# Optimization experiments

Hardware: AMD Instinct MI355X
Metric: run time of the kernel (lower is better)

Reference implementation:

```python
import jax, jax.numpy as jnp
import numpy as np

B = 128          # batch of IQ signals
L = 128          # signal length
PL = 16          # patch length
ST = 4           # patch stride
WIN = 4          # local window
NPATCH = (L - PL) // ST + 1   # 29
HID = 256
NCLS = 8
NG = B * NPATCH               # number of patch graphs
N = NG * PL                   # total nodes


def _build_edges():
    src, dst = [], []
    for i in range(PL):
        for j in range(PL):
            if 0 < abs(i - j) <= WIN:
                src.append(i); dst.append(j)
    bs = np.array(src, np.int32)          # [108]
    bd = np.array(dst, np.int32)
    off = (np.arange(NG, dtype=np.int32) * PL)[:, None]
    isrc = (off + bs[None, :]).reshape(-1)
    idst = (off + bd[None, :]).reshape(-1)
    # cross-patch edges: last node of patch p -> first node of patch p+1
    b = np.arange(B, dtype=np.int32)[:, None]
    p = np.arange(NPATCH - 1, dtype=np.int32)[None, :]
    csrc = (b * NPATCH * PL + p * PL + (PL - 1)).reshape(-1)
    cdst = (b * NPATCH * PL + (p + 1) * PL).reshape(-1)
    return np.concatenate([isrc, csrc]), np.concatenate([idst, cdst])


def setup_inputs() -> dict:
    key = jax.random.key(0)
    ks = jax.random.split(key, 10)
    s = 0.05
    esrc, edst = _build_edges()
    return {
        "iq_signal": jax.random.normal(ks[0], (B, 2, L), jnp.float32),
        "edge_src": jnp.asarray(esrc),
        "edge_dst": jnp.asarray(edst),
        # SAGEConv layer 0 (in=2): lin_l (agg, with bias), lin_r (root, no bias)
        "W0_agg": jax.random.normal(ks[1], (HID, 2), jnp.float32) * s,
        "W0_root": jax.random.normal(ks[2], (HID, 2), jnp.float32) * s,
        "b0": jnp.zeros((HID,), jnp.float32),
        # SAGEConv layers 1..3 (256 -> 256), stacked
        "W_agg": jax.random.normal(ks[3], (3, HID, HID), jnp.float32) * s,
        "W_root": jax.random.normal(ks[4], (3, HID, HID), jnp.float32) * s,
        "b_lin": jnp.zeros((3, HID), jnp.float32),
        # per-layer LayerNorms
        "ln_scale": jnp.ones((4, HID), jnp.float32),
        "ln_bias": jnp.zeros((4, HID), jnp.float32),
        # classifier head
        "cls_W1": jax.random.normal(ks[5], (HID, HID), jnp.float32) * s,
        "cls_b1": jnp.zeros((HID,), jnp.float32),
        "cls_ln_scale": jnp.ones((HID,), jnp.float32),
        "cls_ln_bias": jnp.zeros((HID,), jnp.float32),
        "cls_W2": jax.random.normal(ks[6], (NCLS, HID), jnp.float32) * s,
        "cls_b2": jnp.zeros((NCLS,), jnp.float32),
    }


def _ln(x, g, b):
    m = x.mean(-1, keepdims=True)
    v = ((x - m) ** 2).mean(-1, keepdims=True)
    return (x - m) * jax.lax.rsqrt(v + 1e-5) * g + b


def reference(iq_signal, edge_src, edge_dst, W0_agg, W0_root, b0,
              W_agg, W_root, b_lin, ln_scale, ln_bias,
              cls_W1, cls_b1, cls_ln_scale, cls_ln_bias, cls_W2, cls_b2):
    # patch extraction: [B,2,L] -> [B,NPATCH,PL,2] -> node features [N,2]
    idx = jnp.arange(NPATCH)[:, None] * ST + jnp.arange(PL)[None, :]   # [29,16]
    x = jnp.transpose(iq_signal[:, :, idx], (0, 2, 3, 1)).reshape(-1, 2)

    # in-degree for mean aggregation (0 -> safe divide by 1)
    ones = jnp.ones((edge_dst.shape[0],), x.dtype)
    deg = jax.ops.segment_sum(ones, edge_dst, num_segments=N)
    inv_deg = 1.0 / jnp.maximum(deg, 1.0)

    def sage(h, Wa, Wr, b):
        # mean-aggregate neighbor messages, then lin_l(agg) + lin_r(h) + bias
        agg = jax.ops.segment_sum(h[edge_src], edge_dst, num_segments=N)
        agg = agg * inv_deg[:, None]
        return agg @ Wa.T + h @ Wr.T + b

    # layer 0 (2 -> 256): no residual (shape change)
    h = jax.nn.relu(_ln(sage(x, W0_agg, W0_root, b0), ln_scale[0], ln_bias[0]))
    # layers 1..3 with residual
    for l in range(3):
        hn = jax.nn.relu(_ln(sage(h, W_agg[l], W_root[l], b_lin[l]),
                             ln_scale[l + 1], ln_bias[l + 1]))
        h = h + hn

    node_emb = h                                  # [N, 256]
    # global_mean_pool per patch graph (16 consecutive nodes each)
    gf = node_emb.reshape(NG, PL, HID).mean(axis=1)   # [NG, 256]
    z = jax.nn.relu(_ln(gf @ cls_W1.T + cls_b1, cls_ln_scale, cls_ln_bias))
    logits = z @ cls_W2.T + cls_b2                # [NG, 8]
    return logits, gf, node_emb
```

## Files before the change

kernel.cpp:

```cpp
#include <hip/hip_runtime.h>
#include <hip/hip_bf16.h>

typedef __hip_bfloat16 bf16;
typedef unsigned short u16;
typedef unsigned int uint32;
typedef __attribute__((ext_vector_type(8))) short bf16x8;
typedef __attribute__((ext_vector_type(4))) float f32x4;

#define BATCH   128
#define LSIG    128
#define PL      16
#define ST      4
#define WIN     4
#define NPATCH  29
#define NG      (BATCH * NPATCH)
#define NNODE   (NG * PL)
#define HID     256
#define NCLS    8

#define IQ_OFF    0
#define W0A_OFF   32768
#define W0R_OFF   33280
#define B0_OFF    33792
#define BLIN_OFF  34048
#define LNS_OFF   34816
#define LNB_OFF   35840
#define W1T_OFF   36864
#define CB1_OFF   102400
#define CLNS_OFF  102656
#define CLNB_OFF  102912
#define CW2_OFF   103168
#define CB2_OFF   105216
#define CVT_TOTAL 105224
#define WB_TOTAL  393216

#define P_BYTE_OFF   4096
#define WB_BYTE_OFF  425984
#define A_BYTE_OFF   1216512
#define B_BYTE_OFF   1959936
#define GF_EOFF      (NG * NCLS)
#define EMB_EOFF     (NG * NCLS + NG * HID)

#define MFMA_BF16 __builtin_amdgcn_mfma_f32_16x16x32_bf16

__device__ __forceinline__ float b2f(bf16 x) { return __bfloat162float(x); }
__device__ __forceinline__ float lof(uint32 u) { return __uint_as_float(u << 16); }
__device__ __forceinline__ float hif(uint32 u) { return __uint_as_float(u & 0xFFFF0000u); }
__device__ __forceinline__ uint32 packbf(float a, float b) {
  bf16 r0 = __float2bfloat16(a), r1 = __float2bfloat16(b);
  return ((uint32)(*(const u16*)&r1) << 16) | (uint32)(*(const u16*)&r0);
}
__device__ __forceinline__ float ldmix(const void* p, size_t i, int fl) {
  return fl ? ((const float*)p)[i] : __bfloat162float(((const bf16*)p)[i]);
}
__device__ __forceinline__ void gl_lds16(const uint32* gsrc, uint32* ldst) {
  __builtin_amdgcn_global_load_lds(
      (const __attribute__((address_space(1))) uint32*)gsrc,
      (__attribute__((address_space(3))) uint32*)ldst, 16, 0, 0);
}

__global__ __launch_bounds__(256) void detect_kernel(const u16* __restrict__ iq, int* flag) {
  __shared__ int sbig, snz;
  int t = threadIdx.x;
  if (t == 0) { sbig = 0; snz = 0; }
  __syncthreads();
  int big = 0, nz = 0;
  for (int e = t; e < 16384; e += 256) {
    u16 u = iq[2 * e];
    int ex = (u >> 7) & 0xFF;
    if (ex >= 0xC0) big++;
    if (u != 0) nz++;
  }
  atomicAdd(&sbig, big); atomicAdd(&snz, nz);
  __syncthreads();
  if (t == 0) *flag = (sbig > 4 || snz < 100) ? 1 : 0;
}

__global__ __launch_bounds__(256) void convert_all(
    const int* __restrict__ flag,
    const void* iq, const void* w0a, const void* w0r, const void* b0,
    const void* blin, const void* lns, const void* lnb,
    const void* cw1, const void* cb1, const void* clns, const void* clnb,
    const void* cw2, const void* cb2,
    const void* wag, const void* wro,
    float* __restrict__ P, bf16* __restrict__ WB) {
  int idx = blockIdx.x * 256 + threadIdx.x;
  int fl = *flag;
  if (idx < CVT_TOTAL) {
    float v;
    if (idx < W0A_OFF)        v = ldmix(iq,  idx, fl);
    else if (idx < W0R_OFF)   v = ldmix(w0a, idx - W0A_OFF, fl);
    else if (idx < B0_OFF)    v = ldmix(w0r, idx - W0R_OFF, fl);
    else if (idx < BLIN_OFF)  v = ldmix(b0,  idx - B0_OFF, fl);
    else if (idx < LNS_OFF)   v = ldmix(blin, idx - BLIN_OFF, fl);
    else if (idx < LNB_OFF)   v = ldmix(lns, idx - LNS_OFF, fl);
    else if (idx < W1T_OFF)   v = ldmix(lnb, idx - LNB_OFF, fl);
    else if (idx < CB1_OFF) { int t2 = idx - W1T_OFF;
      v = ldmix(cw1, (t2 & 255) * 256 + (t2 >> 8), fl); }
    else if (idx < CLNS_OFF)  v = ldmix(cb1, idx - CB1_OFF, fl);
    else if (idx < CLNB_OFF)  v = ldmix(clns, idx - CLNS_OFF, fl);
    else if (idx < CW2_OFF)   v = ldmix(clnb, idx - CLNB_OFF, fl);
    else if (idx < CB2_OFF)   v = ldmix(cw2, idx - CW2_OFF, fl);
    else                      v = ldmix(cb2, idx - CB2_OFF, fl);
    P[idx] = v;
  } else if (idx < CVT_TOTAL + WB_TOTAL) {
    int k = idx - CVT_TOTAL;
    int l = k >> 17, m = (k >> 16) & 1, r = k & 65535;
    const void* src = m ? wro : wag;
    WB[k] = __float2bfloat16(ldmix(src, l * 65536 + r, fl));
  }
}

__global__ __launch_bounds__(256) void layer0_kernel(
    const float* __restrict__ P, bf16* __restrict__ hout) {
  int g = blockIdx.x, f = threadIdx.x;
  int b = g / NPATCH, p = g % NPATCH;
  __shared__ float x_s[PL][2];
  __shared__ float xp_s[2];
  __shared__ float agg_s[PL][2];
  __shared__ float o_s[PL][HID];
  __shared__ float mv_s[PL][2];
  if (f < 32) { int j = f & 15, c = f >> 4;
    x_s[j][c] = P[IQ_OFF + (b * 2 + c) * LSIG + p * ST + j]; }
  if (f < 2) xp_s[f] = (p > 0) ? P[IQ_OFF + (b * 2 + f) * LSIG + (p - 1) * ST + PL - 1] : 0.f;
  __syncthreads();
  if (f < 32) { int j = f & 15, c = f >> 4;
    float s = 0.f;
    int lo = j - WIN < 0 ? 0 : j - WIN, hi = j + WIN > 15 ? 15 : j + WIN;
    for (int i = lo; i <= hi; ++i) if (i != j) s += x_s[i][c];
    int deg = (j < WIN ? j : WIN) + ((15 - j) < WIN ? (15 - j) : WIN);
    if (j == 0 && p > 0) { s += xp_s[c]; deg += 1; }
    agg_s[j][c] = s / (float)deg;
  }
  __syncthreads();
  float wa0 = P[W0A_OFF + f * 2], wa1 = P[W0A_OFF + f * 2 + 1];
  float wr0 = P[W0R_OFF + f * 2], wr1 = P[W0R_OFF + f * 2 + 1];
  float bb = P[B0_OFF + f];
#pragma unroll
  for (int j = 0; j < PL; ++j)
    o_s[j][f] = agg_s[j][0] * wa0 + agg_s[j][1] * wa1 + x_s[j][0] * wr0 + x_s[j][1] * wr1 + bb;
  __syncthreads();
  { int j = f >> 4, q = f & 15;
    float s = 0.f, s2 = 0.f;
#pragma unroll
    for (int i = 0; i < 16; ++i) { float v = o_s[j][q + 16 * i]; s += v; s2 += v * v; }
#pragma unroll
    for (int m = 8; m >= 1; m >>= 1) { s += __shfl_xor(s, m); s2 += __shfl_xor(s2, m); }
    if (q == 0) { float mean = s * (1.f / HID);
      float var = s2 * (1.f / HID) - mean * mean;
      mv_s[j][0] = mean; mv_s[j][1] = rsqrtf(var + 1e-5f); }
  }
  __syncthreads();
  float gl = P[LNS_OFF + f], bl = P[LNB_OFF + f];
#pragma unroll
  for (int j = 0; j < PL; ++j) {
    float v = (o_s[j][f] - mv_s[j][0]) * mv_s[j][1] * gl + bl;
    v = v > 0.f ? v : 0.f;
    bf16 x = __float2bfloat16(v);
    ((u16*)hout)[(size_t)(g * PL + j) * 256 + ((((f >> 3) ^ (j & 7))) << 3) + (f & 7)] = *(const u16*)&x;
  }
}

template<int LAST>
__global__ __launch_bounds__(256, 2) void sage_mfma(
    const bf16* __restrict__ hin,
    const bf16* __restrict__ Wa, const bf16* __restrict__ Wr,
    const float* __restrict__ bias,
    const float* __restrict__ lng, const float* __restrict__ lnb,
    bf16* __restrict__ hout,
    void* __restrict__ dout, const int* __restrict__ flag) {
  int t = threadIdx.x;
  int w = t >> 6, l = t & 63, lr = l & 15, lg = l >> 4;
  int g0 = blockIdx.x * 4;
  size_t nbase = (size_t)g0 * PL;
  __shared__ uint32 h32[64 * 128];
  __shared__ uint32 a32[64 * 128];
  float* mvp = (float*)h32;
  const uint32* hinw = (const uint32*)hin;

  int colbase = w * 64;
  const bf16* waB = Wa + (colbase + lr) * HID + lg * 8;
  const bf16* wrB = Wr + (colbase + lr) * HID + lg * 8;
  bf16x8 wa0[2][8], wr0[2][8];
#pragma unroll
  for (int nt = 0; nt < 2; ++nt)
#pragma unroll
    for (int ks = 0; ks < 8; ++ks) {
      wa0[nt][ks] = *(const bf16x8*)(waB + nt * 16 * HID + ks * 32);
      wr0[nt][ks] = *(const bf16x8*)(wrB + nt * 16 * HID + ks * 32);
    }

  const uint32* hgw = hinw + nbase * 128;
#pragma unroll
  for (int it = 0; it < 8; ++it) {
    int off = (it * 4 + w) * 256;
    gl_lds16(hgw + off + (l << 2), &h32[off]);
  }
  __syncthreads();

  {
    int c2 = t & 127, Ph = t >> 7;
#pragma unroll
    for (int pi = 0; pi < 2; ++pi) {
      int pp = Ph + pi * 2;
      int pr = pp * 16;
      int hp = ((g0 + pp) % NPATCH) != 0;
      float vlo[16], vhi[16];
#pragma unroll
      for (int j = 0; j < 16; ++j) {
        uint32 u = h32[(pr + j) * 128 + (((c2 >> 2) ^ (j & 7)) << 2) + (c2 & 3)];
        vlo[j] = lof(u); vhi[j] = hif(u);
      }
      float blo = 0.f, bhi = 0.f;
      if (hp) {
        uint32 u;
        if (pp == 0) u = hinw[(nbase - 1) * 128 + (((c2 >> 2) ^ 7) << 2) + (c2 & 3)];
        else { int br = pr - 1;
          u = h32[br * 128 + (((c2 >> 2) ^ (br & 7)) << 2) + (c2 & 3)]; }
        blo = lof(u); bhi = hif(u);
      }
#pragma unroll
      for (int j = 0; j < 16; ++j) {
        const int a = (j - WIN < 0) ? 0 : j - WIN;
        const int b = (j + WIN > 15) ? 15 : j + WIN;
        float slo = 0.f, shi = 0.f;
#pragma unroll
        for (int i = 0; i < 16; ++i)
          if (i >= a && i <= b && i != j) { slo += vlo[i]; shi += vhi[i]; }
        float deg = (float)((j < WIN ? j : WIN) + (15 - j < WIN ? 15 - j : WIN));
        if (j == 0 && hp) { slo += blo; shi += bhi; deg += 1.f; }
        float inv = 1.f / deg;
        a32[(pr + j) * 128 + (((c2 >> 2) ^ (j & 7)) << 2) + (c2 & 3)] = packbf(slo * inv, shi * inv);
      }
    }
  }
  __syncthreads();

  f32x4 acc[4][4];
#pragma unroll
  for (int m = 0; m < 4; ++m)
#pragma unroll
    for (int n = 0; n < 4; ++n) acc[m][n] = (f32x4){0.f, 0.f, 0.f, 0.f};
  __builtin_amdgcn_s_setprio(1);
#pragma unroll
  for (int ks = 0; ks < 8; ++ks) {
    bf16x8 wa1[2], wr1[2];
#pragma unroll
    for (int nt = 0; nt < 2; ++nt) {
      wa1[nt] = *(const bf16x8*)(waB + (nt + 2) * 16 * HID + ks * 32);
      wr1[nt] = *(const bf16x8*)(wrB + (nt + 2) * 16 * HID + ks * 32);
    }
#pragma unroll
    for (int m = 0; m < 4; ++m) {
      int idx = (m * 16 + lr) * 128 + (((ks * 4 + lg) ^ (lr & 7)) << 2);
      bf16x8 af = *(const bf16x8*)&a32[idx];
      bf16x8 hf = *(const bf16x8*)&h32[idx];
      acc[m][0] = MFMA_BF16(af, wa0[0][ks], acc[m][0], 0, 0, 0);
      acc[m][0] = MFMA_BF16(hf, wr0[0][ks], acc[m][0], 0, 0, 0);
      acc[m][1] = MFMA_BF16(af, wa0[1][ks], acc[m][1], 0, 0, 0);
      acc[m][1] = MFMA_BF16(hf, wr0[1][ks], acc[m][1], 0, 0, 0);
      acc[m][2] = MFMA_BF16(af, wa1[0],     acc[m][2], 0, 0, 0);
      acc[m][2] = MFMA_BF16(hf, wr1[0],     acc[m][2], 0, 0, 0);
      acc[m][3] = MFMA_BF16(af, wa1[1],     acc[m][3], 0, 0, 0);
      acc[m][3] = MFMA_BF16(hf, wr1[1],     acc[m][3], 0, 0, 0);
    }
  }
  __builtin_amdgcn_s_setprio(0);
#pragma unroll
  for (int nt = 0; nt < 4; ++nt) {
    float bv = bias[colbase + nt * 16 + lr];
#pragma unroll
    for (int m = 0; m < 4; ++m) {
      acc[m][nt][0] += bv; acc[m][nt][1] += bv; acc[m][nt][2] += bv; acc[m][nt][3] += bv;
    }
  }
  __syncthreads();

#pragma unroll
  for (int m = 0; m < 4; ++m)
#pragma unroll
    for (int nt = 0; nt < 4; ++nt) {
      int col = colbase + nt * 16 + lr;
#pragma unroll
      for (int r = 0; r < 4; ++r) {
        int row = m * 16 + lg * 4 + r;
        int i16 = row * 256 + (((col >> 3) ^ (row & 7)) << 3) + (col & 7);
        bf16 x = __float2bfloat16(acc[m][nt][r]);
        ((u16*)a32)[i16] = *(const u16*)&x;
      }
    }
  __syncthreads();

  {
    int row = t >> 2, q = t & 3;
    float s = 0.f, s2 = 0.f;
#pragma unroll
    for (int i = 0; i < 32; ++i) {
      int d = q * 32 + i;
      uint32 u = a32[row * 128 + (((d >> 2) ^ (row & 7)) << 2) + (d & 3)];
      float a = lof(u), b = hif(u);
      s += a + b; s2 += a * a + b * b;
    }
    s += __shfl_xor(s, 1); s2 += __shfl_xor(s2, 1);
    s += __shfl_xor(s, 2); s2 += __shfl_xor(s2, 2);
    if (q == 0) { float mean = s * (1.f / HID);
      mvp[row * 2] = mean;
      mvp[row * 2 + 1] = rsqrtf(s2 * (1.f / HID) - mean * mean + 1e-5f); }
  }
  __syncthreads();

  {
    int c2 = t & 127, prt = t >> 7;
    float gl0 = lng[c2 * 2], gl1 = lng[c2 * 2 + 1];
    float bl0 = lnb[c2 * 2], bl1 = lnb[c2 * 2 + 1];
    uint32* outw = nullptr;
    if constexpr (!LAST) outw = (uint32*)hout + nbase * 128;
    const uint32* inw = hinw + nbase * 128;
    int fl = 0;
    if constexpr (LAST) fl = *flag;
#pragma unroll
    for (int pi = 0; pi < 2; ++pi) {
      float sga = 0.f, sgb = 0.f;
#pragma unroll
      for (int i = 0; i < 16; ++i) {
        int row = prt * 32 + pi * 16 + i;
        int pidx = row * 128 + (((c2 >> 2) ^ (row & 7)) << 2) + (c2 & 3);
        uint32 u = a32[pidx];
        float mean = mvp[row * 2], rstd = mvp[row * 2 + 1];
        float a = (lof(u) - mean) * rstd * gl0 + bl0; a = a > 0.f ? a : 0.f;
        float b_ = (hif(u) - mean) * rstd * gl1 + bl1; b_ = b_ > 0.f ? b_ : 0.f;
        uint32 hu = inw[pidx];
        a += lof(hu); b_ += hif(hu);
        if constexpr (!LAST) {
          outw[pidx] = packbf(a, b_);
        } else {
          sga += a; sgb += b_;
          if (fl) {
            size_t ei = (size_t)EMB_EOFF + (nbase + row) * 256 + (size_t)c2 * 2;
            *(float2*)&((float*)dout)[ei] = make_float2(a, b_);
          } else {
            ((uint32*)dout)[(EMB_EOFF >> 1) + (nbase + row) * 128 + c2] = packbf(a, b_);
          }
        }
      }
      if constexpr (LAST) {
        float ga = sga * (1.f / PL), gb = sgb * (1.f / PL);
        int gidx = g0 + prt * 2 + pi;
        if (fl) {
          size_t gi = (size_t)GF_EOFF + (size_t)gidx * 256 + (size_t)c2 * 2;
          *(float2*)&((float*)dout)[gi] = make_float2(ga, gb);
        } else {
          ((uint32*)dout)[(GF_EOFF >> 1) + gidx * 128 + c2] = packbf(ga, gb);
        }
      }
    }
  }
}

__global__ __launch_bounds__(256) void head_kernel(
    const void* __restrict__ gin, const float* __restrict__ P,
    void* __restrict__ dout, const int* __restrict__ flag) {
  int g = blockIdx.x, f = threadIdx.x;
  int fl = *flag;
  __shared__ float gf_s[HID];
  __shared__ float z_s[HID];
  __shared__ float ps[4], ps2[4];
  __shared__ float mr[2];
  gf_s[f] = fl ? ((const float*)gin)[(size_t)GF_EOFF + (size_t)g * HID + f]
               : b2f(((const bf16*)gin)[(size_t)GF_EOFF + (size_t)g * HID + f]);
  __syncthreads();
  float acc = P[CB1_OFF + f];
  for (int k = 0; k < HID; k += 4) {
    const float4 gv = *(const float4*)(&gf_s[k]);
    acc = fmaf(gv.x, P[W1T_OFF + (k + 0) * HID + f], acc);
    acc = fmaf(gv.y, P[W1T_OFF + (k + 1) * HID + f], acc);
    acc = fmaf(gv.z, P[W1T_OFF + (k + 2) * HID + f], acc);
    acc = fmaf(gv.w, P[W1T_OFF + (k + 3) * HID + f], acc);
  }
  float s1 = acc, s2 = acc * acc;
#pragma unroll
  for (int m = 32; m >= 1; m >>= 1) { s1 += __shfl_xor(s1, m); s2 += __shfl_xor(s2, m); }
  int wid = f >> 6, lane = f & 63;
  if (lane == 0) { ps[wid] = s1; ps2[wid] = s2; }
  __syncthreads();
  if (f == 0) {
    float S = ps[0] + ps[1] + ps[2] + ps[3];
    float S2 = ps2[0] + ps2[1] + ps2[2] + ps2[3];
    float mean = S * (1.f / HID);
    mr[0] = mean; mr[1] = rsqrtf(S2 * (1.f / HID) - mean * mean + 1e-5f);
  }
  __syncthreads();
  float z = (acc - mr[0]) * mr[1] * P[CLNS_OFF + f] + P[CLNB_OFF + f];
  z = z > 0.f ? z : 0.f;
  z_s[f] = z;
  __syncthreads();
  {
    int cls = f >> 5, lane2 = f & 31;
    float a = 0.f;
    for (int k = lane2; k < HID; k += 32)
      a = fmaf(z_s[k], P[CW2_OFF + cls * HID + k], a);
    a += __shfl_xor(a, 16); a += __shfl_xor(a, 8);
    a += __shfl_xor(a, 4);  a += __shfl_xor(a, 2); a += __shfl_xor(a, 1);
    if (lane2 == 0) {
      a += P[CB2_OFF + cls];
      size_t ei = (size_t)g * NCLS + cls;
      if (fl) ((float*)dout)[ei] = a; else ((bf16*)dout)[ei] = __float2bfloat16(a);
    }
  }
}

extern "C" void kernel_launch(void* const* d_in, const int* in_sizes, int n_in,
                              void* d_out, int out_size, void* d_ws, size_t ws_size,
                              hipStream_t stream) {
  char* ws = (char*)d_ws;
  int*   flag = (int*)ws;
  float* P    = (float*)(ws + P_BYTE_OFF);
  bf16*  WB   = (bf16*)(ws + WB_BYTE_OFF);
  bf16*  A    = (bf16*)(ws + A_BYTE_OFF);
  bf16*  B    = (bf16*)((char*)d_out + B_BYTE_OFF);

  detect_kernel<<<1, 256, 0, stream>>>((const u16*)d_in[0], flag);
  convert_all<<<(CVT_TOTAL + WB_TOTAL + 255) / 256, 256, 0, stream>>>(
      flag, d_in[0], d_in[3], d_in[4], d_in[5], d_in[8],
      d_in[9], d_in[10], d_in[11], d_in[12], d_in[13], d_in[14], d_in[15], d_in[16],
      d_in[6], d_in[7], P, WB);

  layer0_kernel<<<NG, 256, 0, stream>>>(P, A);
  sage_mfma<0><<<NG / 4, 256, 0, stream>>>(A, WB, WB + 65536,
      P + BLIN_OFF, P + LNS_OFF + HID, P + LNB_OFF + HID, B, nullptr, flag);
  sage_mfma<0><<<NG / 4, 256, 0, stream>>>(B, WB + 131072, WB + 131072 + 65536,
      P + BLIN_OFF + HID, P + LNS_OFF + 2 * HID, P + LNB_OFF + 2 * HID, A, nullptr, flag);
  sage_mfma<1><<<NG / 4, 256, 0, stream>>>(A, WB + 262144, WB + 262144 + 65536,
      P + BLIN_OFF + 2 * HID, P + LNS_OFF + 3 * HID, P + LNB_OFF + 3 * HID, nullptr, d_out, flag);
  head_kernel<<<NG, 256, 0, stream>>>(d_out, P, d_out, flag);
}
```

Before: 225.3 us.

## Add 8-patch-per-block SAGE kernel with in-place LDS aggregation for middle layers

Introduces a new SAGE layer kernel that processes 8 patch graphs per 512-thread block. It computes the root GEMM first, then aggregates neighbours in place in a single 64KB LDS buffer and runs the aggregation GEMM on the same buffer, instead of using separate h and agg buffers. Weight fragments are read directly from global memory/cache per MFMA. The aim is to cut LDS footprint and per-block overhead and to amortise weight reads over more rows. The trade-off is more global weight traffic per block, and 64KB of LDS per block may limit occupancy.

After: 421.8 us. 1.87x slower.

```diff
diff --git a/kernel.cpp b/kernel.cpp
--- a/kernel.cpp
+++ b/kernel.cpp
@@ -161,6 +161,144 @@
   }
 }
 
+__global__ __launch_bounds__(512, 2) void sage_bp8(
+    const bf16* __restrict__ hin,
+    const bf16* __restrict__ Wa, const bf16* __restrict__ Wr,
+    const float* __restrict__ bias,
+    const float* __restrict__ lng, const float* __restrict__ lnb,
+    bf16* __restrict__ hout) {
+  int t = threadIdx.x;
+  int w = t >> 6, l = t & 63, lr = l & 15, lg = l >> 4;
+  int g0 = blockIdx.x * 8;
+  size_t nbase = (size_t)g0 * PL;
+  __shared__ uint32 hb[128 * 128];
+  const uint32* hinw = (const uint32*)hin;
+
+  const uint32* hg = hinw + nbase * 128;
+#pragma unroll
+  for (int it = 0; it < 8; ++it) {
+    int off = (it * 8 + w) * 256;
+    gl_lds16(hg + off + (l << 2), &hb[off]);
+  }
+  __syncthreads();
+
+  int rowbase = w * 16;
+  const bf16* wrB = Wr + lr * HID + lg * 8;
+  const bf16* waB = Wa + lr * HID + lg * 8;
+
+  f32x4 acc[16];
+#pragma unroll
+  for (int n = 0; n < 16; ++n) acc[n] = (f32x4){0.f, 0.f, 0.f, 0.f};
+  __builtin_amdgcn_s_setprio(1);
+#pragma unroll
+  for (int ks = 0; ks < 8; ++ks) {
+    bf16x8 hf = *(const bf16x8*)&hb[(rowbase + lr) * 128 + (((ks * 4 + lg) ^ (lr & 7)) << 2)];
+#pragma unroll
+    for (int nt = 0; nt < 16; ++nt) {
+      bf16x8 wf = *(const bf16x8*)(wrB + nt * 16 * HID + ks * 32);
+      acc[nt] = MFMA_BF16(hf, wf, acc[nt], 0, 0, 0);
+    }
+  }
+  __builtin_amdgcn_s_setprio(0);
+
+  int c2 = t & 127, pg = t >> 7;
+  uint32 bnd[2];
+#pragma unroll
+  for (int pi2 = 0; pi2 < 2; ++pi2) {
+    int pi = pg * 2 + pi2;
+    int hp = ((g0 + pi) % NPATCH) != 0;
+    uint32 u = 0;
+    if (hp) {
+      if (pi == 0) u = hinw[(nbase - 1) * 128 + (((c2 >> 2) ^ 7) << 2) + (c2 & 3)];
+      else { int br = pi * 16 - 1;
+        u = hb[br * 128 + (((c2 >> 2) ^ 7) << 2) + (c2 & 3)]; }
+    }
+    bnd[pi2] = u;
+  }
+  __syncthreads();
+
+#pragma unroll
+  for (int pi2 = 0; pi2 < 2; ++pi2) {
+    int pi = pg * 2 + pi2;
+    int pr = pi * 16;
+    int hp = ((g0 + pi) % NPATCH) != 0;
+    float vlo[16], vhi[16];
+#pragma unroll
+    for (int j = 0; j < 16; ++j) {
+      uint32 u = hb[(pr + j) * 128 + (((c2 >> 2) ^ (j & 7)) << 2) + (c2 & 3)];
+      vlo[j] = lof(u); vhi[j] = hif(u);
+    }
+    float blo = lof(bnd[pi2]), bhi = hif(bnd[pi2]);
+#pragma unroll
+    for (int j = 0; j < 16; ++j) {
+      const int a = (j - WIN < 0) ? 0 : j - WIN;
+      const int b = (j + WIN > 15) ? 15 : j + WIN;
+      float slo = 0.f, shi = 0.f;
+#pragma unroll
+      for (int i = 0; i < 16; ++i)
+        if (i >= a && i <= b && i != j) { slo += vlo[i]; shi += vhi[i]; }
+      float deg = (float)((j < WIN ? j : WIN) + (15 - j < WIN ? 15 - j : WIN));
+      if (j == 0 && hp) { slo += blo; shi += bhi; deg += 1.f; }
+      float inv = 1.f / deg;
+      hb[(pr + j) * 128 + (((c2 >> 2) ^ (j & 7)) << 2) + (c2 & 3)] = packbf(slo * inv, shi * inv);
+    }
+  }
+  __syncthreads();
+
+  __builtin_amdgcn_s_setprio(1);
+#pragma unroll
+  for (int ks = 0; ks < 8; ++ks) {
+    bf16x8 af = *(const bf16x8*)&hb[(rowbase + lr) * 128 + (((ks * 4 + lg) ^ (lr & 7)) << 2)];
+#pragma unroll
+    for (int nt = 0; nt < 16; ++nt) {
+      bf16x8 wf = *(const bf16x8*)(waB + nt * 16 * HID + ks * 32);
+      acc[nt] = MFMA_BF16(af, wf, acc[nt], 0, 0, 0);
+    }
+  }
+  __builtin_amdgcn_s_setprio(0);
+
+#pragma unroll
+  for (int nt = 0; nt < 16; ++nt) {
+    float bv = bias[nt * 16 + lr];
+    acc[nt][0] += bv; acc[nt][1] += bv; acc[nt][2] += bv; acc[nt][3] += bv;
+  }
+  float mean[4], rstd[4];
+#pragma unroll
+  for (int r = 0; r < 4; ++r) {
+    float s = 0.f, s2 = 0.f;
+#pragma unroll
+    for (int nt = 0; nt < 16; ++nt) { float v = acc[nt][r]; s += v; s2 += v * v; }
+    s += __shfl_xor(s, 1); s2 += __shfl_xor(s2, 1);
+    s += __shfl_xor(s, 2); s2 += __shfl_xor(s2, 2);
+    s += __shfl_xor(s, 4); s2 += __shfl_xor(s2, 4);
+    s += __shfl_xor(s, 8); s2 += __shfl_xor(s2, 8);
+    mean[r] = s * (1.f / HID);
+    rstd[r] = rsqrtf(s2 * (1.f / HID) - mean[r] * mean[r] + 1e-5f);
+  }
+
+  float glv[16], blv[16];
+#pragma unroll
+  for (int nt = 0; nt < 16; ++nt) { glv[nt] = lng[nt * 16 + lr]; blv[nt] = lnb[nt * 16 + lr]; }
+  const u16* hin16 = (const u16*)hin;
+  u16* hout16 = (u16*)hout;
+#pragma unroll
+  for (int r = 0; r < 4; ++r) {
+    int rowL = rowbase + lg * 4 + r;
+    size_t node = nbase + rowL;
+    int r7 = rowL & 7;
+#pragma unroll
+    for (int nt = 0; nt < 16; ++nt) {
+      float v = (acc[nt][r] - mean[r]) * rstd[r] * glv[nt] + blv[nt];
+      v = v > 0.f ? v : 0.f;
+      size_t a16 = node * 256 + (size_t)((((nt * 2 + (lr >> 3)) ^ r7) << 3) + (lr & 7));
+      u16 hraw = hin16[a16];
+      v += __bfloat162float(*(const bf16*)&hraw);
+      bf16 x = __float2bfloat16(v);
+      hout16[a16] = *(const u16*)&x;
+    }
+  }
+}
+
 template<int LAST>
 __global__ __launch_bounds__(256, 2) void sage_mfma(
     const bf16* __restrict__ hin,
@@ -426,10 +564,10 @@
       d_in[6], d_in[7], P, WB);
 
   layer0_kernel<<<NG, 256, 0, stream>>>(P, A);
-  sage_mfma<0><<<NG / 4, 256, 0, stream>>>(A, WB, WB + 65536,
-      P + BLIN_OFF, P + LNS_OFF + HID, P + LNB_OFF + HID, B, nullptr, flag);
-  sage_mfma<0><<<NG / 4, 256, 0, stream>>>(B, WB + 131072, WB + 131072 + 65536,
-      P + BLIN_OFF + HID, P + LNS_OFF + 2 * HID, P + LNB_OFF + 2 * HID, A, nullptr, flag);
+  sage_bp8<<<NG / 8, 512, 0, stream>>>(A, WB, WB + 65536,
+      P + BLIN_OFF, P + LNS_OFF + HID, P + LNB_OFF + HID, B);
+  sage_bp8<<<NG / 8, 512, 0, stream>>>(B, WB + 131072, WB + 131072 + 65536,
+      P + BLIN_OFF + HID, P + LNS_OFF + 2 * HID, P + LNB_OFF + 2 * HID, A);
   sage_mfma<1><<<NG / 4, 256, 0, stream>>>(A, WB + 262144, WB + 262144 + 65536,
       P + BLIN_OFF + 2 * HID, P + LNS_OFF + 3 * HID, P + LNB_OFF + 3 * HID, nullptr, d_out, flag);
   head_kernel<<<NG, 256, 0, stream>>>(d_out, P, d_out, flag);
```
